# Kernel tuning notes

Measured on AMD Instinct MI355X. Metric: run time of the kernel, lower is better.

## Reference

```python
import jax, jax.numpy as jnp
import numpy as np

B, T, C = 4, 2048, 2048
H = 16
D = C // H  # head_dim = 128
THETA = 10000.0


def rope_cos_sin(t, d, dtype=jnp.float32):
    inv_freq = 1.0 / (THETA ** (jnp.arange(0, d, 2, dtype=jnp.float32) / d))  # [D/2]
    pos = jnp.arange(t, dtype=jnp.float32)
    freqs = jnp.outer(pos, inv_freq)                 # [T, D/2]
    emb = jnp.concatenate([freqs, freqs], axis=-1)   # [T, D]
    return jnp.cos(emb).astype(dtype), jnp.sin(emb).astype(dtype)


def rotate_half(x):
    x1, x2 = jnp.split(x, 2, axis=-1)
    return jnp.concatenate([-x2, x1], axis=-1)


def setup_inputs() -> dict:
    key = jax.random.key(0)
    k1, k2, k3 = jax.random.split(key, 3)
    x = jax.random.normal(k1, (B, T, C), dtype=jnp.float32)
    Wqkv = jax.random.normal(k2, (C, 3 * C), dtype=jnp.float32) * (1.0 / np.sqrt(C))
    Wout = jax.random.normal(k3, (C, C), dtype=jnp.float32) * (1.0 / np.sqrt(C))
    return {"x": x, "Wqkv": Wqkv, "Wout": Wout}


def reference(x, Wqkv, Wout):
    b, t, c = x.shape
    qkv = jnp.einsum('btc,cd->btd', x, Wqkv)          # [B,T,3C]
    q, k, v = jnp.split(qkv, 3, axis=-1)
    # [B,T,C] -> [B,H,T,D]
    q = q.reshape(b, t, H, D).transpose(0, 2, 1, 3)
    k = k.reshape(b, t, H, D).transpose(0, 2, 1, 3)
    v = v.reshape(b, t, H, D).transpose(0, 2, 1, 3)
    cos, sin = rope_cos_sin(t, D, x.dtype)            # [T,D]
    cos = cos[None, None]                             # [1,1,T,D]
    sin = sin[None, None]
    q = q * cos + rotate_half(q) * sin
    k = k * cos + rotate_half(k) * sin
    scale = 1.0 / np.sqrt(D)
    scores = jnp.einsum('bhqd,bhkd->bhqk', q, k) * scale
    causal = jnp.tril(jnp.ones((t, t), dtype=bool))
    scores = jnp.where(causal[None, None], scores, jnp.finfo(scores.dtype).min)
    attn = jax.nn.softmax(scores, axis=-1)
    y = jnp.einsum('bhqk,bhkd->bhqd', attn, v)        # [B,H,T,D]
    y = y.transpose(0, 2, 1, 3).reshape(b, t, c)      # [B,T,C]
    return jnp.einsum('btc,cd->btd', y, Wout)
```

## Files before the change

kernel.cpp:

```cpp
#include <hip/hip_runtime.h>
#include <hip/hip_bf16.h>
#include <cmath>

#define Bsz   4
#define Tlen  2048
#define Cdim  2048
#define Hn    16
#define Dh    128
#define N_QKV 6144
#define Mrows 8192

typedef __bf16 bf16x8 __attribute__((ext_vector_type(8)));
typedef __bf16 bf16x4 __attribute__((ext_vector_type(4)));
typedef float  f32x4  __attribute__((ext_vector_type(4)));
typedef uint32_t u32x2 __attribute__((ext_vector_type(2)));

__device__ __forceinline__ f32x4 mfma16(bf16x8 a, bf16x8 b, f32x4 c) {
  return __builtin_amdgcn_mfma_f32_16x16x32_bf16(a, b, c, 0, 0, 0);
}

__device__ __forceinline__ void gl16(const void* g, void* l) {
  __builtin_amdgcn_global_load_lds(
      (const __attribute__((address_space(1))) void*)g,
      (__attribute__((address_space(3))) void*)l, 16, 0, 0);
}

__device__ __forceinline__ uint32_t pack_bf16(float lo, float hi) {
  union { __bf16 h; unsigned short u; } a, b;
  a.h = (__bf16)lo; b.h = (__bf16)hi;
  return (uint32_t)a.u | ((uint32_t)b.u << 16);
}

__global__ void rope_table_k(float* __restrict__ cosT, float* __restrict__ sinT) {
  int idx = blockIdx.x * 256 + threadIdx.x;
  int t = idx >> 6, i = idx & 63;
  float invf = __expf(-(float)i * 0.14391156698f);
  float a = (float)t * invf;
  float s, c;
  sincosf(a, &s, &c);
  cosT[idx] = c;
  sinT[idx] = s;
}

__global__ __launch_bounds__(256) void f32_to_bf16_k(
    const float* __restrict__ src, __bf16* __restrict__ dst) {
  size_t i = ((size_t)blockIdx.x * 256 + threadIdx.x) * 8;
  f32x4 a = *(const f32x4*)(src + i);
  f32x4 b = *(const f32x4*)(src + i + 4);
  bf16x8 o;
  o[0] = (__bf16)a[0]; o[1] = (__bf16)a[1]; o[2] = (__bf16)a[2]; o[3] = (__bf16)a[3];
  o[4] = (__bf16)b[0]; o[5] = (__bf16)b[1]; o[6] = (__bf16)b[2]; o[7] = (__bf16)b[3];
  *(bf16x8*)(dst + i) = o;
}

__global__ __launch_bounds__(256) void transpose_to_bf16_k(
    const float* __restrict__ src, __bf16* __restrict__ dst, int K, int N) {
  __shared__ float tile[32][33];
  int n0 = blockIdx.x * 32, k0 = blockIdx.y * 32;
  int tr = threadIdx.x >> 3, tc = (threadIdx.x & 7) * 4;
  f32x4 v = *(const f32x4*)&src[(size_t)(k0 + tr) * N + n0 + tc];
  tile[tr][tc + 0] = v[0]; tile[tr][tc + 1] = v[1];
  tile[tr][tc + 2] = v[2]; tile[tr][tc + 3] = v[3];
  __syncthreads();
  bf16x4 w;
  w[0] = (__bf16)tile[tc + 0][tr];
  w[1] = (__bf16)tile[tc + 1][tr];
  w[2] = (__bf16)tile[tc + 2][tr];
  w[3] = (__bf16)tile[tc + 3][tr];
  *(bf16x4*)&dst[(size_t)(n0 + tr) * K + k0 + tc] = w;
}

__global__ __launch_bounds__(512, 2) void qkv_gemm(
    const __bf16* __restrict__ Xb, const __bf16* __restrict__ Wt,
    __bf16* __restrict__ Qo, __bf16* __restrict__ Ko, __bf16* __restrict__ Vo,
    const float* __restrict__ cosT, const float* __restrict__ sinT)
{
  __shared__ union SM {
    struct { __bf16 A[2][256 * 64]; __bf16 B[2][256 * 64]; } s;
    float C[64][265];
  } sm;

  const int tid = threadIdx.x, lane = tid & 63, wid = tid >> 6;
  const int g = lane >> 4, l16 = lane & 15;
  const int wr = wid >> 2, wc = wid & 3;

  const int bid = blockIdx.x;
  const int xcd = bid & 7, idx = bid >> 3;
  const int stl = idx >> 4, pos = idx & 15;
  const int m0 = (xcd * 4 + (pos >> 2)) * 256;
  const int n0 = (stl * 4 + (pos & 3)) * 256;

  const int srow = tid >> 3;
  const int schk = (tid & 7) ^ (srow & 7);
  const __bf16* gA = Xb + (size_t)(m0 + srow) * Cdim + schk * 8;
  const __bf16* gB = Wt + (size_t)(n0 + srow) * Cdim + schk * 8;
  const int ldst = wid * 512;

  f32x4 acc[8][4] = {};
  const int NT = Cdim / 64;

  #pragma unroll
  for (int r = 0; r < 4; ++r) {
    gl16(gA + (size_t)r * 64 * Cdim, &sm.s.A[0][r * 4096 + ldst]);
    gl16(gB + (size_t)r * 64 * Cdim, &sm.s.B[0][r * 4096 + ldst]);
  }
  #pragma unroll
  for (int r = 0; r < 4; ++r) {
    gl16(gA + 64 + (size_t)r * 64 * Cdim, &sm.s.A[1][r * 4096 + ldst]);
    gl16(gB + 64 + (size_t)r * 64 * Cdim, &sm.s.B[1][r * 4096 + ldst]);
  }

  for (int t = 0; t < NT; ++t) {
    const int p = t & 1;
    if (t < NT - 1) asm volatile("s_waitcnt vmcnt(8)" ::: "memory");
    else            asm volatile("s_waitcnt vmcnt(0)" ::: "memory");
    __builtin_amdgcn_s_barrier();
    __builtin_amdgcn_sched_barrier(0);

    #pragma unroll
    for (int kk = 0; kk < 2; ++kk) {
      bf16x8 a[8], b[4];
      const int ch = (((kk << 2) | g) ^ (l16 & 7)) * 8;
      #pragma unroll
      for (int f = 0; f < 8; ++f)
        a[f] = *(const bf16x8*)&sm.s.A[p][(wr * 128 + f * 16 + l16) * 64 + ch];
      #pragma unroll
      for (int n = 0; n < 4; ++n)
        b[n] = *(const bf16x8*)&sm.s.B[p][(wc * 64 + n * 16 + l16) * 64 + ch];
      #pragma unroll
      for (int f = 0; f < 8; ++f)
        #pragma unroll
        for (int n = 0; n < 4; ++n)
          acc[f][n] = mfma16(a[f], b[n], acc[f][n]);
    }

    __builtin_amdgcn_sched_barrier(0);
    asm volatile("s_waitcnt lgkmcnt(0)" ::: "memory");
    __builtin_amdgcn_s_barrier();

    if (t + 2 < NT) {
      const __bf16* pA = gA + (size_t)(t + 2) * 64;
      const __bf16* pB = gB + (size_t)(t + 2) * 64;
      #pragma unroll
      for (int r = 0; r < 4; ++r) {
        gl16(pA + (size_t)r * 64 * Cdim, &sm.s.A[p][r * 4096 + ldst]);
        gl16(pB + (size_t)r * 64 * Cdim, &sm.s.B[p][r * 4096 + ldst]);
      }
    }
  }

  const int sel = n0 >> 11;
  const int h0  = (n0 & 2047) >> 7;
  const int erow = tid >> 3, q = tid & 7;
  const int dlo = (q & 3) * 16;
  const int clo = (q >> 2) * 128 + dlo;
  const int vcol = tid >> 1, vth = tid & 1;

  #pragma unroll
  for (int rh = 0; rh < 4; ++rh) {
    if (wr == (rh >> 1)) {
      const int fb = (rh & 1) * 4;
      #pragma unroll
      for (int f2 = 0; f2 < 4; ++f2)
        #pragma unroll
        for (int n = 0; n < 4; ++n)
          #pragma unroll
          for (int r = 0; r < 4; ++r)
            sm.C[f2 * 16 + g * 4 + r][wc * 64 + n * 16 + l16] = acc[fb + f2][n][r];
    }
    __syncthreads();
    if (sel == 2) {
      const int hh = h0 + (vcol >> 7), d = vcol & 127;
      const int mb = m0 + rh * 64 + vth * 32;
      const int b_ = mb >> 11, tt = mb & 2047;
      __bf16* outp = Vo + (((size_t)(b_ * Hn + hh)) * Dh + d) * Tlen + tt;
      bf16x8 w[4];
      #pragma unroll
      for (int i = 0; i < 32; ++i)
        w[i >> 3][i & 7] = (__bf16)sm.C[vth * 32 + i][vcol];
      #pragma unroll
      for (int k = 0; k < 4; ++k) *(bf16x8*)&outp[k * 8] = w[k];
    } else {
      __bf16* dst = (sel == 0) ? Qo : Ko;
      const int m = m0 + rh * 64 + erow;
      const int b_ = m >> 11, t = m & 2047;
      __bf16* out = dst + (((size_t)(b_ * Hn + h0 + (q >> 2))) * Tlen + t) * Dh + dlo;
      const float* cb = cosT + t * 64 + dlo;
      const float* sb = sinT + t * 64 + dlo;
      bf16x8 o1[2], o2[2];
      #pragma unroll
      for (int i = 0; i < 16; ++i) {
        float v1 = sm.C[erow][clo + i];
        float v2 = sm.C[erow][clo + i + 64];
        float cs = cb[i], sn = sb[i];
        float r1 = v1 * cs - v2 * sn;
        float r2 = v2 * cs + v1 * sn;
        o1[i >> 3][i & 7] = (__bf16)r1;
        o2[i >> 3][i & 7] = (__bf16)r2;
      }
      *(bf16x8*)&out[0]  = o1[0];
      *(bf16x8*)&out[8]  = o1[1];
      *(bf16x8*)&out[64] = o2[0];
      *(bf16x8*)&out[72] = o2[1];
    }
    __syncthreads();
  }
}

__global__ __launch_bounds__(256, 2) void attn_fwd(
    const __bf16* __restrict__ Qg, const __bf16* __restrict__ Kg,
    const __bf16* __restrict__ Vtg, __bf16* __restrict__ Yg)
{
  __shared__ __bf16 Ks[2][64 * 128];
  __shared__ __bf16 Vt[2][128 * 64];
  __shared__ uint32_t Ps2[4][16 * 34 + 2];

  const int tid = threadIdx.x, lane = tid & 63, wid = tid >> 6;
  const int g = lane >> 4, l16 = lane & 15;
  const int qt = gridDim.x - 1 - blockIdx.x;
  const int q0 = qt * 64;
  const size_t bh = (size_t)blockIdx.z * Hn + blockIdx.y;
  const __bf16* Kbase = Kg + bh * ((size_t)Tlen * Dh);
  const __bf16* Vbase = Vtg + bh * ((size_t)Dh * Tlen);

  const int q_glob = q0 + wid * 16 + l16;

  bf16x8 aq[4];
  {
    const __bf16* qrow = Qg + (bh * Tlen + q_glob) * Dh;
    #pragma unroll
    for (int ks = 0; ks < 4; ++ks)
      aq[ks] = *(const bf16x8*)(qrow + ks * 32 + 8 * g);
  }

  float m_r = -1e30f, l_r = 0.f;
  f32x4 o[8] = {};
  const float k_e = 0.08838834764831845f * 1.4426950408889634f;

  const int NKV = qt + 1;

  const int krow = lane >> 4, kchk = lane & 15;
  const int vrow = lane >> 3, vchk = lane & 7;

#define STAGE_KV(kv0_, buf_)                                                    \
  {                                                                             \
    _Pragma("unroll")                                                           \
    for (int rr = 0; rr < 4; ++rr) {                                            \
      const int row = wid * 16 + rr * 4 + krow;                                 \
      const int sc = kchk ^ (row & 7);                                          \
      gl16(Kbase + (size_t)((kv0_) + row) * Dh + sc * 8,                        \
           &Ks[buf_][(wid * 16 + rr * 4) * 128]);                               \
    }                                                                           \
    _Pragma("unroll")                                                           \
    for (int rr = 0; rr < 4; ++rr) {                                            \
      const int row = wid * 32 + rr * 8 + vrow;                                 \
      const int sc = vchk ^ (row & 7);                                          \
      gl16(Vbase + (size_t)row * Tlen + (kv0_) + sc * 8,                        \
           &Vt[buf_][(wid * 32 + rr * 8) * 64]);                                \
    }                                                                           \
  }

  STAGE_KV(0, 0);

  for (int it = 0; it < NKV; ++it) {
    const int p = it & 1;
    if (it + 1 < NKV) {
      STAGE_KV((it + 1) * 64, (it + 1) & 1);
      asm volatile("s_waitcnt vmcnt(8)" ::: "memory");
    } else {
      asm volatile("s_waitcnt vmcnt(0)" ::: "memory");
    }
    __builtin_amdgcn_s_barrier();
    __builtin_amdgcn_sched_barrier(0);

    f32x4 s[4] = {};
    __builtin_amdgcn_s_setprio(1);
    #pragma unroll
    for (int ks = 0; ks < 4; ++ks) {
      const int ch = ((4 * ks + g) ^ (l16 & 7)) * 8;
      #pragma unroll
      for (int nf = 0; nf < 4; ++nf) {
        bf16x8 bk = *(const bf16x8*)&Ks[p][(nf * 16 + l16) * 128 + ch];
        s[nf] = mfma16(bk, aq[ks], s[nf]);
      }
    }
    __builtin_amdgcn_s_setprio(0);

    if (it == qt) {
      const int kvb = it * 64 + 4 * g;
      #pragma unroll
      for (int nf = 0; nf < 4; ++nf)
        #pragma unroll
        for (int r = 0; r < 4; ++r)
          if (kvb + nf * 16 + r > q_glob) s[nf][r] = -1e30f;
    }

    float mx = s[0][0];
    #pragma unroll
    for (int nf = 0; nf < 4; ++nf)
      #pragma unroll
      for (int r = 0; r < 4; ++r) mx = fmaxf(mx, s[nf][r]);
    mx = fmaxf(mx, __shfl_xor(mx, 16, 64));
    mx = fmaxf(mx, __shfl_xor(mx, 32, 64));

    if (__any(mx > m_r)) {
      const float mn = fmaxf(m_r, mx);
      const float al = exp2f((m_r - mn) * k_e);
      m_r = mn;
      l_r *= al;
      #pragma unroll
      for (int n2 = 0; n2 < 8; ++n2)
        #pragma unroll
        for (int r = 0; r < 4; ++r) o[n2][r] *= al;
    }

    const float mk = -m_r * k_e;
    float rs = 0.f;
    #pragma unroll
    for (int nf = 0; nf < 4; ++nf)
      #pragma unroll
      for (int r = 0; r < 4; ++r) {
        const float pv = exp2f(fmaf(s[nf][r], k_e, mk));
        s[nf][r] = pv;
        rs += pv;
      }
    rs += __shfl_xor(rs, 16, 64);
    rs += __shfl_xor(rs, 32, 64);
    l_r += rs;

    #pragma unroll
    for (int nf = 0; nf < 4; ++nf) {
      u32x2 wv;
      wv.x = pack_bf16(s[nf][0], s[nf][1]);
      wv.y = pack_bf16(s[nf][2], s[nf][3]);
      *(u32x2*)&Ps2[wid][l16 * 34 + nf * 8 + 2 * g] = wv;
    }
    asm volatile("s_waitcnt lgkmcnt(0)" ::: "memory");
    __builtin_amdgcn_sched_barrier(0);

    union { u32x2 h[2]; bf16x8 v; } pb0, pb1;
    pb0.h[0] = *(const u32x2*)&Ps2[wid][l16 * 34 + 4 * g];
    pb0.h[1] = *(const u32x2*)&Ps2[wid][l16 * 34 + 4 * g + 2];
    pb1.h[0] = *(const u32x2*)&Ps2[wid][l16 * 34 + 16 + 4 * g];
    pb1.h[1] = *(const u32x2*)&Ps2[wid][l16 * 34 + 16 + 4 * g + 2];

    const int c0 = (g ^ (l16 & 7)) * 8;
    const int c1 = ((4 + g) ^ (l16 & 7)) * 8;
    __builtin_amdgcn_s_setprio(1);
    #pragma unroll
    for (int n2 = 0; n2 < 8; ++n2) {
      bf16x8 vb0 = *(const bf16x8*)&Vt[p][(n2 * 16 + l16) * 64 + c0];
      bf16x8 vb1 = *(const bf16x8*)&Vt[p][(n2 * 16 + l16) * 64 + c1];
      o[n2] = mfma16(vb0, pb0.v, o[n2]);
      o[n2] = mfma16(vb1, pb1.v, o[n2]);
    }
    __builtin_amdgcn_s_setprio(0);

    asm volatile("s_waitcnt lgkmcnt(0)" ::: "memory");
    __builtin_amdgcn_sched_barrier(0);
    __builtin_amdgcn_s_barrier();
  }
#undef STAGE_KV

  const float inv = 1.0f / l_r;
  __bf16* yrow = Yg + ((size_t)(blockIdx.z * Tlen + q0 + wid * 16 + l16)) * Cdim
               + blockIdx.y * Dh;
  #pragma unroll
  for (int n2 = 0; n2 < 8; ++n2) {
    bf16x4 w;
    #pragma unroll
    for (int r = 0; r < 4; ++r) w[r] = (__bf16)(o[n2][r] * inv);
    *(bf16x4*)&yrow[n2 * 16 + 4 * g] = w;
  }
}

__global__ __launch_bounds__(512, 2) void out_gemm(
    const __bf16* __restrict__ Yb, const __bf16* __restrict__ Wt,
    float* __restrict__ O)
{
  __shared__ struct { __bf16 A[2][256 * 64]; __bf16 B[2][256 * 64]; } sm;

  const int tid = threadIdx.x, lane = tid & 63, wid = tid >> 6;
  const int g = lane >> 4, l16 = lane & 15;
  const int wr = wid >> 2, wc = wid & 3;

  const int bid = blockIdx.x;
  const int xcd = bid & 7, idx = bid >> 3;
  const int stl = idx >> 4, pos = idx & 15;
  const int m0 = (xcd * 4 + (pos >> 2)) * 256;
  const int n0 = (stl * 4 + (pos & 3)) * 256;

  const int srow = tid >> 3;
  const int schk = (tid & 7) ^ (srow & 7);
  const __bf16* gA = Yb + (size_t)(m0 + srow) * Cdim + schk * 8;
  const __bf16* gB = Wt + (size_t)(n0 + srow) * Cdim + schk * 8;
  const int ldst = wid * 512;

  f32x4 acc[8][4] = {};
  const int NT = Cdim / 64;

  #pragma unroll
  for (int r = 0; r < 4; ++r) {
    gl16(gA + (size_t)r * 64 * Cdim, &sm.A[0][r * 4096 + ldst]);
    gl16(gB + (size_t)r * 64 * Cdim, &sm.B[0][r * 4096 + ldst]);
  }
  #pragma unroll
  for (int r = 0; r < 4; ++r) {
    gl16(gA + 64 + (size_t)r * 64 * Cdim, &sm.A[1][r * 4096 + ldst]);
    gl16(gB + 64 + (size_t)r * 64 * Cdim, &sm.B[1][r * 4096 + ldst]);
  }

  for (int t = 0; t < NT; ++t) {
    const int p = t & 1;
    if (t < NT - 1) asm volatile("s_waitcnt vmcnt(8)" ::: "memory");
    else            asm volatile("s_waitcnt vmcnt(0)" ::: "memory");
    __builtin_amdgcn_s_barrier();
    __builtin_amdgcn_sched_barrier(0);

    #pragma unroll
    for (int kk = 0; kk < 2; ++kk) {
      bf16x8 a[8], b[4];
      const int ch = (((kk << 2) | g) ^ (l16 & 7)) * 8;
      #pragma unroll
      for (int f = 0; f < 8; ++f)
        a[f] = *(const bf16x8*)&sm.A[p][(wr * 128 + f * 16 + l16) * 64 + ch];
      #pragma unroll
      for (int n = 0; n < 4; ++n)
        b[n] = *(const bf16x8*)&sm.B[p][(wc * 64 + n * 16 + l16) * 64 + ch];
      #pragma unroll
      for (int f = 0; f < 8; ++f)
        #pragma unroll
        for (int n = 0; n < 4; ++n)
          acc[f][n] = mfma16(a[f], b[n], acc[f][n]);
    }

    __builtin_amdgcn_sched_barrier(0);
    asm volatile("s_waitcnt lgkmcnt(0)" ::: "memory");
    __builtin_amdgcn_s_barrier();

    if (t + 2 < NT) {
      const __bf16* pA = gA + (size_t)(t + 2) * 64;
      const __bf16* pB = gB + (size_t)(t + 2) * 64;
      #pragma unroll
      for (int r = 0; r < 4; ++r) {
        gl16(pA + (size_t)r * 64 * Cdim, &sm.A[p][r * 4096 + ldst]);
        gl16(pB + (size_t)r * 64 * Cdim, &sm.B[p][r * 4096 + ldst]);
      }
    }
  }

  #pragma unroll
  for (int f = 0; f < 8; ++f)
    #pragma unroll
    for (int n = 0; n < 4; ++n)
      #pragma unroll
      for (int r = 0; r < 4; ++r)
        O[(size_t)(m0 + wr * 128 + f * 16 + g * 4 + r) * Cdim
          + (n0 + wc * 64 + n * 16 + l16)] = acc[f][n][r];
}

extern "C" void kernel_launch(void* const* d_in, const int* in_sizes, int n_in,
                              void* d_out, int out_size, void* d_ws, size_t ws_size,
                              hipStream_t stream) {
  const float* x    = (const float*)d_in[0];
  const float* Wqkv = (const float*)d_in[1];
  const float* Wout = (const float*)d_in[2];
  float* out = (float*)d_out;

  float*  cosT   = (float*)d_ws;
  float*  sinT   = cosT + Tlen * 64;
  __bf16* Xb     = (__bf16*)(sinT + Tlen * 64);
  __bf16* Wqkv_t = Xb + (size_t)Mrows * Cdim;
  __bf16* Wout_t = Wqkv_t + (size_t)N_QKV * Cdim;
  __bf16* Qb     = Wout_t + (size_t)Cdim * Cdim;
  __bf16* Kb     = Qb + (size_t)Bsz * Hn * Tlen * Dh;
  __bf16* Vb     = Kb + (size_t)Bsz * Hn * Tlen * Dh;
  __bf16* Yb     = Xb;

  rope_table_k<<<dim3(512), dim3(256), 0, stream>>>(cosT, sinT);
  f32_to_bf16_k<<<dim3(Mrows * Cdim / (256 * 8)), dim3(256), 0, stream>>>(x, Xb);
  transpose_to_bf16_k<<<dim3(N_QKV / 32, Cdim / 32), dim3(256), 0, stream>>>(
      Wqkv, Wqkv_t, Cdim, N_QKV);
  transpose_to_bf16_k<<<dim3(Cdim / 32, Cdim / 32), dim3(256), 0, stream>>>(
      Wout, Wout_t, Cdim, Cdim);
  qkv_gemm<<<dim3(768), dim3(512), 0, stream>>>(
      Xb, Wqkv_t, Qb, Kb, Vb, cosT, sinT);
  attn_fwd<<<dim3(Tlen / 64, Hn, Bsz), dim3(256), 0, stream>>>(Qb, Kb, Vb, Yb);
  out_gemm<<<dim3(256), dim3(512), 0, stream>>>(Yb, Wout_t, out);
}
```

Baseline: 670.0 us.

## Split GEMM k-tiles into quadrant phases with interleaved loads and MFMA priority

Both the QKV and output GEMMs now break each 64-wide k-tile into four sub-phases over quadrants of the 256x256 output tile. Each phase issues a quarter of the next tile's global-to-LDS loads, reads its A/B fragments, and runs its MFMAs under raised wave priority (s_setprio). The aim is to overlap memory traffic and LDS reads with matrix math more finely than the old whole-tile loop, and to lower register pressure from fragment arrays. In exchange it adds more barriers per k-tile, and the hand-scheduled vmcnt counts must line up exactly with the staged loads.

Measured after the change: 1.276 ms. 1.91x slower.

```diff
diff --git a/kernel.cpp b/kernel.cpp
--- a/kernel.cpp
+++ b/kernel.cpp
@@ -30,6 +30,51 @@
   a.h = (__bf16)lo; b.h = (__bf16)hi;
   return (uint32_t)a.u | ((uint32_t)b.u << 16);
 }
+
+union GemmSM {
+  struct { __bf16 A[2][256 * 64]; __bf16 B[2][256 * 64]; } s;
+  float C[64][265];
+};
+
+#define STAGE_A(buf_, k0_, mq_) {                                             \
+  _Pragma("unroll") for (int rnd_ = 0; rnd_ < 2; ++rnd_) {                    \
+    const int lr_ = rnd_ * 128 + (mq_) * 64 + (wid << 3);                     \
+    gl16(gA0 + (size_t)lr_ * Cdim + (k0_), &sm.s.A[buf_][lr_ * 64]);          \
+  } }
+#define STAGE_B(buf_, k0_, nq_) {                                             \
+  _Pragma("unroll") for (int rnd_ = 0; rnd_ < 2; ++rnd_) {                    \
+    const int lr_ = rnd_ * 128 + (nq_) * 32 + ((wid >> 2) << 6)               \
+                  + ((wid & 3) << 3);                                         \
+    gl16(gB0 + (size_t)lr_ * Cdim + (k0_), &sm.s.B[buf_][lr_ * 64]);          \
+  } }
+#define PHASE(buf_, mq_, nq_, VM_, STAGE_)                                    \
+  {                                                                           \
+    bf16x8 a_[4][2], b_[2][2];                                                \
+    _Pragma("unroll") for (int kk = 0; kk < 2; ++kk) {                        \
+      const int ch_ = (((kk << 2) | g) ^ (l16 & 7)) * 8;                      \
+      _Pragma("unroll") for (int fq = 0; fq < 4; ++fq)                        \
+        a_[fq][kk] = *(const bf16x8*)                                         \
+          &sm.s.A[buf_][(wr * 128 + (mq_) * 64 + fq * 16 + l16) * 64 + ch_];  \
+      _Pragma("unroll") for (int nn = 0; nn < 2; ++nn)                        \
+        b_[nn][kk] = *(const bf16x8*)                                         \
+          &sm.s.B[buf_][(wc * 64 + (nq_) * 32 + nn * 16 + l16) * 64 + ch_];   \
+    }                                                                         \
+    STAGE_                                                                    \
+    __builtin_amdgcn_s_barrier();                                             \
+    asm volatile("s_waitcnt lgkmcnt(0)" ::: "memory");                        \
+    __builtin_amdgcn_sched_barrier(0);                                        \
+    __builtin_amdgcn_s_setprio(1);                                            \
+    _Pragma("unroll") for (int kk = 0; kk < 2; ++kk)                          \
+      _Pragma("unroll") for (int fq = 0; fq < 4; ++fq)                        \
+        _Pragma("unroll") for (int nn = 0; nn < 2; ++nn)                      \
+          acc[(mq_) * 4 + fq][(nq_) * 2 + nn] =                               \
+            mfma16(a_[fq][kk], b_[nn][kk], acc[(mq_) * 4 + fq][(nq_) * 2 + nn]); \
+    __builtin_amdgcn_s_setprio(0);                                            \
+    __builtin_amdgcn_sched_barrier(0);                                        \
+    asm volatile("s_waitcnt vmcnt(" VM_ ")" ::: "memory");                    \
+    __builtin_amdgcn_s_barrier();                                             \
+    __builtin_amdgcn_sched_barrier(0);                                        \
+  }
 
 __global__ void rope_table_k(float* __restrict__ cosT, float* __restrict__ sinT) {
   int idx = blockIdx.x * 256 + threadIdx.x;
@@ -75,10 +120,7 @@
     __bf16* __restrict__ Qo, __bf16* __restrict__ Ko, __bf16* __restrict__ Vo,
     const float* __restrict__ cosT, const float* __restrict__ sinT)
 {
-  __shared__ union SM {
-    struct { __bf16 A[2][256 * 64]; __bf16 B[2][256 * 64]; } s;
-    float C[64][265];
-  } sm;
+  __shared__ GemmSM sm;
 
   const int tid = threadIdx.x, lane = tid & 63, wid = tid >> 6;
   const int g = lane >> 4, l16 = lane & 15;
@@ -90,63 +132,38 @@
   const int m0 = (xcd * 4 + (pos >> 2)) * 256;
   const int n0 = (stl * 4 + (pos & 3)) * 256;
 
-  const int srow = tid >> 3;
-  const int schk = (tid & 7) ^ (srow & 7);
-  const __bf16* gA = Xb + (size_t)(m0 + srow) * Cdim + schk * 8;
-  const __bf16* gB = Wt + (size_t)(n0 + srow) * Cdim + schk * 8;
-  const int ldst = wid * 512;
+  const int schk = (lane & 7) ^ ((lane >> 3) & 7);
+  const __bf16* gA0 = Xb + (size_t)(m0 + (lane >> 3)) * Cdim + schk * 8;
+  const __bf16* gB0 = Wt + (size_t)(n0 + (lane >> 3)) * Cdim + schk * 8;
 
   f32x4 acc[8][4] = {};
-  const int NT = Cdim / 64;
-
-  #pragma unroll
-  for (int r = 0; r < 4; ++r) {
-    gl16(gA + (size_t)r * 64 * Cdim, &sm.s.A[0][r * 4096 + ldst]);
-    gl16(gB + (size_t)r * 64 * Cdim, &sm.s.B[0][r * 4096 + ldst]);
-  }
-  #pragma unroll
-  for (int r = 0; r < 4; ++r) {
-    gl16(gA + 64 + (size_t)r * 64 * Cdim, &sm.s.A[1][r * 4096 + ldst]);
-    gl16(gB + 64 + (size_t)r * 64 * Cdim, &sm.s.B[1][r * 4096 + ldst]);
-  }
-
-  for (int t = 0; t < NT; ++t) {
-    const int p = t & 1;
-    if (t < NT - 1) asm volatile("s_waitcnt vmcnt(8)" ::: "memory");
-    else            asm volatile("s_waitcnt vmcnt(0)" ::: "memory");
-    __builtin_amdgcn_s_barrier();
-    __builtin_amdgcn_sched_barrier(0);
-
-    #pragma unroll
-    for (int kk = 0; kk < 2; ++kk) {
-      bf16x8 a[8], b[4];
-      const int ch = (((kk << 2) | g) ^ (l16 & 7)) * 8;
-      #pragma unroll
-      for (int f = 0; f < 8; ++f)
-        a[f] = *(const bf16x8*)&sm.s.A[p][(wr * 128 + f * 16 + l16) * 64 + ch];
-      #pragma unroll
-      for (int n = 0; n < 4; ++n)
-        b[n] = *(const bf16x8*)&sm.s.B[p][(wc * 64 + n * 16 + l16) * 64 + ch];
-      #pragma unroll
-      for (int f = 0; f < 8; ++f)
-        #pragma unroll
-        for (int n = 0; n < 4; ++n)
-          acc[f][n] = mfma16(a[f], b[n], acc[f][n]);
-    }
-
-    __builtin_amdgcn_sched_barrier(0);
-    asm volatile("s_waitcnt lgkmcnt(0)" ::: "memory");
-    __builtin_amdgcn_s_barrier();
-
-    if (t + 2 < NT) {
-      const __bf16* pA = gA + (size_t)(t + 2) * 64;
-      const __bf16* pB = gB + (size_t)(t + 2) * 64;
-      #pragma unroll
-      for (int r = 0; r < 4; ++r) {
-        gl16(pA + (size_t)r * 64 * Cdim, &sm.s.A[p][r * 4096 + ldst]);
-        gl16(pB + (size_t)r * 64 * Cdim, &sm.s.B[p][r * 4096 + ldst]);
-      }
-    }
+
+  STAGE_A(0, 0, 0) STAGE_B(0, 0, 0) STAGE_A(0, 0, 1) STAGE_B(0, 0, 1)
+  asm volatile("s_waitcnt vmcnt(4)" ::: "memory");
+  __builtin_amdgcn_s_barrier();
+  __builtin_amdgcn_sched_barrier(0);
+
+  for (int I = 0; I < 15; ++I) {
+    const int t1k = (2 * I + 1) * 64, t2k = (2 * I + 2) * 64;
+    PHASE(0, 0, 0, "4", STAGE_A(1, t1k, 0))
+    PHASE(0, 1, 0, "4", STAGE_B(1, t1k, 0))
+    PHASE(0, 0, 1, "4", STAGE_A(1, t1k, 1))
+    PHASE(0, 1, 1, "4", STAGE_B(1, t1k, 1))
+    PHASE(1, 0, 0, "4", STAGE_A(0, t2k, 0))
+    PHASE(1, 1, 0, "4", STAGE_B(0, t2k, 0))
+    PHASE(1, 0, 1, "4", STAGE_A(0, t2k, 1))
+    PHASE(1, 1, 1, "4", STAGE_B(0, t2k, 1))
+  }
+  {
+    const int t1k = 31 * 64;
+    PHASE(0, 0, 0, "4", STAGE_A(1, t1k, 0))
+    PHASE(0, 1, 0, "4", STAGE_B(1, t1k, 0))
+    PHASE(0, 0, 1, "4", STAGE_A(1, t1k, 1))
+    PHASE(0, 1, 1, "0", STAGE_B(1, t1k, 1))
+    PHASE(1, 0, 0, "0", )
+    PHASE(1, 1, 0, "0", )
+    PHASE(1, 0, 1, "0", )
+    PHASE(1, 1, 1, "0", )
   }
 
   const int sel = n0 >> 11;
@@ -378,7 +395,7 @@
     const __bf16* __restrict__ Yb, const __bf16* __restrict__ Wt,
     float* __restrict__ O)
 {
-  __shared__ struct { __bf16 A[2][256 * 64]; __bf16 B[2][256 * 64]; } sm;
+  __shared__ GemmSM sm;
 
   const int tid = threadIdx.x, lane = tid & 63, wid = tid >> 6;
   const int g = lane >> 4, l16 = lane & 15;
@@ -390,63 +407,38 @@
   const int m0 = (xcd * 4 + (pos >> 2)) * 256;
   const int n0 = (stl * 4 + (pos & 3)) * 256;
 
-  const int srow = tid >> 3;
-  const int schk = (tid & 7) ^ (srow & 7);
-  const __bf16* gA = Yb + (size_t)(m0 + srow) * Cdim + schk * 8;
-  const __bf16* gB = Wt + (size_t)(n0 + srow) * Cdim + schk * 8;
-  const int ldst = wid * 512;
+  const int schk = (lane & 7) ^ ((lane >> 3) & 7);
+  const __bf16* gA0 = Yb + (size_t)(m0 + (lane >> 3)) * Cdim + schk * 8;
+  const __bf16* gB0 = Wt + (size_t)(n0 + (lane >> 3)) * Cdim + schk * 8;
 
   f32x4 acc[8][4] = {};
-  const int NT = Cdim / 64;
-
-  #pragma unroll
-  for (int r = 0; r < 4; ++r) {
-    gl16(gA + (size_t)r * 64 * Cdim, &sm.A[0][r * 4096 + ldst]);
-    gl16(gB + (size_t)r * 64 * Cdim, &sm.B[0][r * 4096 + ldst]);
-  }
-  #pragma unroll
-  for (int r = 0; r < 4; ++r) {
-    gl16(gA + 64 + (size_t)r * 64 * Cdim, &sm.A[1][r * 4096 + ldst]);
-    gl16(gB + 64 + (size_t)r * 64 * Cdim, &sm.B[1][r * 4096 + ldst]);
-  }
-
-  for (int t = 0; t < NT; ++t) {
-    const int p = t & 1;
-    if (t < NT - 1) asm volatile("s_waitcnt vmcnt(8)" ::: "memory");
-    else            asm volatile("s_waitcnt vmcnt(0)" ::: "memory");
-    __builtin_amdgcn_s_barrier();
-    __builtin_amdgcn_sched_barrier(0);
-
-    #pragma unroll
-    for (int kk = 0; kk < 2; ++kk) {
-      bf16x8 a[8], b[4];
-      const int ch = (((kk << 2) | g) ^ (l16 & 7)) * 8;
-      #pragma unroll
-      for (int f = 0; f < 8; ++f)
-        a[f] = *(const bf16x8*)&sm.A[p][(wr * 128 + f * 16 + l16) * 64 + ch];
-      #pragma unroll
-      for (int n = 0; n < 4; ++n)
-        b[n] = *(const bf16x8*)&sm.B[p][(wc * 64 + n * 16 + l16) * 64 + ch];
-      #pragma unroll
-      for (int f = 0; f < 8; ++f)
-        #pragma unroll
-        for (int n = 0; n < 4; ++n)
-          acc[f][n] = mfma16(a[f], b[n], acc[f][n]);
-    }
-
-    __builtin_amdgcn_sched_barrier(0);
-    asm volatile("s_waitcnt lgkmcnt(0)" ::: "memory");
-    __builtin_amdgcn_s_barrier();
-
-    if (t + 2 < NT) {
-      const __bf16* pA = gA + (size_t)(t + 2) * 64;
-      const __bf16* pB = gB + (size_t)(t + 2) * 64;
-      #pragma unroll
-      for (int r = 0; r < 4; ++r) {
-        gl16(pA + (size_t)r * 64 * Cdim, &sm.A[p][r * 4096 + ldst]);
-        gl16(pB + (size_t)r * 64 * Cdim, &sm.B[p][r * 4096 + ldst]);
-      }
-    }
+
+  STAGE_A(0, 0, 0) STAGE_B(0, 0, 0) STAGE_A(0, 0, 1) STAGE_B(0, 0, 1)
+  asm volatile("s_waitcnt vmcnt(4)" ::: "memory");
+  __builtin_amdgcn_s_barrier();
+  __builtin_amdgcn_sched_barrier(0);
+
+  for (int I = 0; I < 15; ++I) {
+    const int t1k = (2 * I + 1) * 64, t2k = (2 * I + 2) * 64;
+    PHASE(0, 0, 0, "4", STAGE_A(1, t1k, 0))
+    PHASE(0, 1, 0, "4", STAGE_B(1, t1k, 0))
+    PHASE(0, 0, 1, "4", STAGE_A(1, t1k, 1))
+    PHASE(0, 1, 1, "4", STAGE_B(1, t1k, 1))
+    PHASE(1, 0, 0, "4", STAGE_A(0, t2k, 0))
+    PHASE(1, 1, 0, "4", STAGE_B(0, t2k, 0))
+    PHASE(1, 0, 1, "4", STAGE_A(0, t2k, 1))
+    PHASE(1, 1, 1, "4", STAGE_B(0, t2k, 1))
+  }
+  {
+    const int t1k = 31 * 64;
+    PHASE(0, 0, 0, "4", STAGE_A(1, t1k, 0))
+    PHASE(0, 1, 0, "4", STAGE_B(1, t1k, 0))
+    PHASE(0, 0, 1, "4", STAGE_A(1, t1k, 1))
+    PHASE(0, 1, 1, "0", STAGE_B(1, t1k, 1))
+    PHASE(1, 0, 0, "0", )
+    PHASE(1, 1, 0, "0", )
+    PHASE(1, 0, 1, "0", )
+    PHASE(1, 1, 1, "0", )
   }
 
   #pragma unroll
```

## Replace 256x256 double-buffered GEMMs with simpler 128x128 single-buffer tiles

Applied to the files above, without the earlier changes.

Both the QKV and output GEMMs move from 256x256 tiles with 512 threads, a two-stage global_load_lds pipeline and K-step 64 to 128x128 tiles with 256 threads, a single LDS buffer and K-step 32, with a barrier before and after every load. The grids grow to 3072 and 1024 blocks and the RoPE/V-transpose epilogue is remapped to one head per tile. Smaller tiles raise occupancy and parallelism, but they lower arithmetic intensity and remove the load/compute overlap, so the GEMMs become more exposed to memory latency.

Result: slower. 816.7 us (+21.9%).

```diff
diff --git a/kernel.cpp b/kernel.cpp
--- a/kernel.cpp
+++ b/kernel.cpp
@@ -70,110 +70,78 @@
   *(bf16x4*)&dst[(size_t)(n0 + tr) * K + k0 + tc] = w;
 }
 
-__global__ __launch_bounds__(512, 2) void qkv_gemm(
+__global__ __launch_bounds__(256) void qkv_gemm(
     const __bf16* __restrict__ Xb, const __bf16* __restrict__ Wt,
     __bf16* __restrict__ Qo, __bf16* __restrict__ Ko, __bf16* __restrict__ Vo,
     const float* __restrict__ cosT, const float* __restrict__ sinT)
 {
   __shared__ union SM {
-    struct { __bf16 A[2][256 * 64]; __bf16 B[2][256 * 64]; } s;
-    float C[64][265];
+    struct { __bf16 A[128 * 32]; __bf16 B[128 * 32]; } s;
+    float C[64][132];
   } sm;
 
   const int tid = threadIdx.x, lane = tid & 63, wid = tid >> 6;
   const int g = lane >> 4, l16 = lane & 15;
-  const int wr = wid >> 2, wc = wid & 3;
+  const int wr = wid >> 1, wc = wid & 1;
 
   const int bid = blockIdx.x;
   const int xcd = bid & 7, idx = bid >> 3;
-  const int stl = idx >> 4, pos = idx & 15;
-  const int m0 = (xcd * 4 + (pos >> 2)) * 256;
-  const int n0 = (stl * 4 + (pos & 3)) * 256;
-
-  const int srow = tid >> 3;
-  const int schk = (tid & 7) ^ (srow & 7);
-  const __bf16* gA = Xb + (size_t)(m0 + srow) * Cdim + schk * 8;
-  const __bf16* gB = Wt + (size_t)(n0 + srow) * Cdim + schk * 8;
-  const int ldst = wid * 512;
-
-  f32x4 acc[8][4] = {};
-  const int NT = Cdim / 64;
+  const int stl = idx >> 6, pos = idx & 63;
+  const int by = xcd * 8 + (pos >> 3), bx = stl * 8 + (pos & 7);
+  const int m0 = by * 128, n0 = bx * 128;
+
+  const int sr0 = lane >> 2;
+  f32x4 acc[4][4] = {};
+
+  for (int k0 = 0; k0 < Cdim; k0 += 32) {
+    __syncthreads();
+    #pragma unroll
+    for (int j = 0; j < 2; ++j) {
+      const int rr = wid * 32 + j * 16 + sr0;
+      const int sc = (lane & 3) ^ ((rr >> 1) & 3);
+      gl16(Xb + (size_t)(m0 + rr) * Cdim + k0 + sc * 8,
+           &sm.s.A[(wid * 32 + j * 16) * 32]);
+      gl16(Wt + (size_t)(n0 + rr) * Cdim + k0 + sc * 8,
+           &sm.s.B[(wid * 32 + j * 16) * 32]);
+    }
+    __syncthreads();
+
+    bf16x8 a[4], b[4];
+    const int ca = (g ^ ((l16 >> 1) & 3)) * 8;
+    #pragma unroll
+    for (int f = 0; f < 4; ++f) {
+      a[f] = *(const bf16x8*)&sm.s.A[(wr * 64 + f * 16 + l16) * 32 + ca];
+      b[f] = *(const bf16x8*)&sm.s.B[(wc * 64 + f * 16 + l16) * 32 + ca];
+    }
+    #pragma unroll
+    for (int mf = 0; mf < 4; ++mf)
+      #pragma unroll
+      for (int nf = 0; nf < 4; ++nf)
+        acc[mf][nf] = mfma16(a[mf], b[nf], acc[mf][nf]);
+  }
+
+  const int sel = n0 >> 11;
+  const int h   = (n0 & 2047) >> 7;
+  const int erow = tid >> 2, jb = (tid & 3) * 16;
+  const int vcol = tid >> 1, vth = tid & 1;
 
   #pragma unroll
-  for (int r = 0; r < 4; ++r) {
-    gl16(gA + (size_t)r * 64 * Cdim, &sm.s.A[0][r * 4096 + ldst]);
-    gl16(gB + (size_t)r * 64 * Cdim, &sm.s.B[0][r * 4096 + ldst]);
-  }
-  #pragma unroll
-  for (int r = 0; r < 4; ++r) {
-    gl16(gA + 64 + (size_t)r * 64 * Cdim, &sm.s.A[1][r * 4096 + ldst]);
-    gl16(gB + 64 + (size_t)r * 64 * Cdim, &sm.s.B[1][r * 4096 + ldst]);
-  }
-
-  for (int t = 0; t < NT; ++t) {
-    const int p = t & 1;
-    if (t < NT - 1) asm volatile("s_waitcnt vmcnt(8)" ::: "memory");
-    else            asm volatile("s_waitcnt vmcnt(0)" ::: "memory");
-    __builtin_amdgcn_s_barrier();
-    __builtin_amdgcn_sched_barrier(0);
-
-    #pragma unroll
-    for (int kk = 0; kk < 2; ++kk) {
-      bf16x8 a[8], b[4];
-      const int ch = (((kk << 2) | g) ^ (l16 & 7)) * 8;
-      #pragma unroll
-      for (int f = 0; f < 8; ++f)
-        a[f] = *(const bf16x8*)&sm.s.A[p][(wr * 128 + f * 16 + l16) * 64 + ch];
-      #pragma unroll
-      for (int n = 0; n < 4; ++n)
-        b[n] = *(const bf16x8*)&sm.s.B[p][(wc * 64 + n * 16 + l16) * 64 + ch];
-      #pragma unroll
-      for (int f = 0; f < 8; ++f)
+  for (int rh = 0; rh < 2; ++rh) {
+    __syncthreads();
+    if (wr == rh) {
+      #pragma unroll
+      for (int mf = 0; mf < 4; ++mf)
         #pragma unroll
-        for (int n = 0; n < 4; ++n)
-          acc[f][n] = mfma16(a[f], b[n], acc[f][n]);
-    }
-
-    __builtin_amdgcn_sched_barrier(0);
-    asm volatile("s_waitcnt lgkmcnt(0)" ::: "memory");
-    __builtin_amdgcn_s_barrier();
-
-    if (t + 2 < NT) {
-      const __bf16* pA = gA + (size_t)(t + 2) * 64;
-      const __bf16* pB = gB + (size_t)(t + 2) * 64;
-      #pragma unroll
-      for (int r = 0; r < 4; ++r) {
-        gl16(pA + (size_t)r * 64 * Cdim, &sm.s.A[p][r * 4096 + ldst]);
-        gl16(pB + (size_t)r * 64 * Cdim, &sm.s.B[p][r * 4096 + ldst]);
-      }
-    }
-  }
-
-  const int sel = n0 >> 11;
-  const int h0  = (n0 & 2047) >> 7;
-  const int erow = tid >> 3, q = tid & 7;
-  const int dlo = (q & 3) * 16;
-  const int clo = (q >> 2) * 128 + dlo;
-  const int vcol = tid >> 1, vth = tid & 1;
-
-  #pragma unroll
-  for (int rh = 0; rh < 4; ++rh) {
-    if (wr == (rh >> 1)) {
-      const int fb = (rh & 1) * 4;
-      #pragma unroll
-      for (int f2 = 0; f2 < 4; ++f2)
-        #pragma unroll
-        for (int n = 0; n < 4; ++n)
+        for (int nf = 0; nf < 4; ++nf)
           #pragma unroll
           for (int r = 0; r < 4; ++r)
-            sm.C[f2 * 16 + g * 4 + r][wc * 64 + n * 16 + l16] = acc[fb + f2][n][r];
+            sm.C[mf * 16 + g * 4 + r][wc * 64 + nf * 16 + l16] = acc[mf][nf][r];
     }
     __syncthreads();
     if (sel == 2) {
-      const int hh = h0 + (vcol >> 7), d = vcol & 127;
       const int mb = m0 + rh * 64 + vth * 32;
       const int b_ = mb >> 11, tt = mb & 2047;
-      __bf16* outp = Vo + (((size_t)(b_ * Hn + hh)) * Dh + d) * Tlen + tt;
+      __bf16* outp = Vo + (((size_t)(b_ * Hn + h)) * Dh + vcol) * Tlen + tt;
       bf16x8 w[4];
       #pragma unroll
       for (int i = 0; i < 32; ++i)
@@ -184,26 +152,25 @@
       __bf16* dst = (sel == 0) ? Qo : Ko;
       const int m = m0 + rh * 64 + erow;
       const int b_ = m >> 11, t = m & 2047;
-      __bf16* out = dst + (((size_t)(b_ * Hn + h0 + (q >> 2))) * Tlen + t) * Dh + dlo;
-      const float* cb = cosT + t * 64 + dlo;
-      const float* sb = sinT + t * 64 + dlo;
+      __bf16* out = dst + (((size_t)(b_ * Hn + h)) * Tlen + t) * Dh;
+      const float* cb = cosT + t * 64 + jb;
+      const float* sb = sinT + t * 64 + jb;
       bf16x8 o1[2], o2[2];
       #pragma unroll
       for (int i = 0; i < 16; ++i) {
-        float v1 = sm.C[erow][clo + i];
-        float v2 = sm.C[erow][clo + i + 64];
+        float v1 = sm.C[erow][jb + i];
+        float v2 = sm.C[erow][jb + i + 64];
         float cs = cb[i], sn = sb[i];
         float r1 = v1 * cs - v2 * sn;
         float r2 = v2 * cs + v1 * sn;
         o1[i >> 3][i & 7] = (__bf16)r1;
         o2[i >> 3][i & 7] = (__bf16)r2;
       }
-      *(bf16x8*)&out[0]  = o1[0];
-      *(bf16x8*)&out[8]  = o1[1];
-      *(bf16x8*)&out[64] = o2[0];
-      *(bf16x8*)&out[72] = o2[1];
-    }
-    __syncthreads();
+      *(bf16x8*)&out[jb]      = o1[0];
+      *(bf16x8*)&out[jb + 8]  = o1[1];
+      *(bf16x8*)&out[jb + 64] = o2[0];
+      *(bf16x8*)&out[jb + 72] = o2[1];
+    }
   }
 }
 
@@ -374,89 +341,60 @@
   }
 }
 
-__global__ __launch_bounds__(512, 2) void out_gemm(
+__global__ __launch_bounds__(256) void out_gemm(
     const __bf16* __restrict__ Yb, const __bf16* __restrict__ Wt,
     float* __restrict__ O)
 {
-  __shared__ struct { __bf16 A[2][256 * 64]; __bf16 B[2][256 * 64]; } sm;
+  __shared__ struct { __bf16 A[128 * 32]; __bf16 B[128 * 32]; } sm;
 
   const int tid = threadIdx.x, lane = tid & 63, wid = tid >> 6;
   const int g = lane >> 4, l16 = lane & 15;
-  const int wr = wid >> 2, wc = wid & 3;
+  const int wr = wid >> 1, wc = wid & 1;
 
   const int bid = blockIdx.x;
   const int xcd = bid & 7, idx = bid >> 3;
-  const int stl = idx >> 4, pos = idx & 15;
-  const int m0 = (xcd * 4 + (pos >> 2)) * 256;
-  const int n0 = (stl * 4 + (pos & 3)) * 256;
-
-  const int srow = tid >> 3;
-  const int schk = (tid & 7) ^ (srow & 7);
-  const __bf16* gA = Yb + (size_t)(m0 + srow) * Cdim + schk * 8;
-  const __bf16* gB = Wt + (size_t)(n0 + srow) * Cdim + schk * 8;
-  const int ldst = wid * 512;
-
-  f32x4 acc[8][4] = {};
-  const int NT = Cdim / 64;
+  const int stl = idx >> 6, pos = idx & 63;
+  const int by = xcd * 8 + (pos >> 3), bx = stl * 8 + (pos & 7);
+  const int m0 = by * 128, n0 = bx * 128;
+
+  const int sr0 = lane >> 2;
+  f32x4 acc[4][4] = {};
+
+  for (int k0 = 0; k0 < Cdim; k0 += 32) {
+    __syncthreads();
+    #pragma unroll
+    for (int j = 0; j < 2; ++j) {
+      const int rr = wid * 32 + j * 16 + sr0;
+      const int sc = (lane & 3) ^ ((rr >> 1) & 3);
+      gl16(Yb + (size_t)(m0 + rr) * Cdim + k0 + sc * 8,
+           &sm.A[(wid * 32 + j * 16) * 32]);
+      gl16(Wt + (size_t)(n0 + rr) * Cdim + k0 + sc * 8,
+           &sm.B[(wid * 32 + j * 16) * 32]);
+    }
+    __syncthreads();
+
+    bf16x8 a[4], b[4];
+    const int ca = (g ^ ((l16 >> 1) & 3)) * 8;
+    #pragma unroll
+    for (int f = 0; f < 4; ++f) {
+      a[f] = *(const bf16x8*)&sm.A[(wr * 64 + f * 16 + l16) * 32 + ca];
+      b[f] = *(const bf16x8*)&sm.B[(wc * 64 + f * 16 + l16) * 32 + ca];
+    }
+    #pragma unroll
+    for (int mf = 0; mf < 4; ++mf)
+      #pragma unroll
+      for (int nf = 0; nf < 4; ++nf)
+        acc[mf][nf] = mfma16(a[mf], b[nf], acc[mf][nf]);
+  }
 
   #pragma unroll
-  for (int r = 0; r < 4; ++r) {
-    gl16(gA + (size_t)r * 64 * Cdim, &sm.A[0][r * 4096 + ldst]);
-    gl16(gB + (size_t)r * 64 * Cdim, &sm.B[0][r * 4096 + ldst]);
-  }
-  #pragma unroll
-  for (int r = 0; r < 4; ++r) {
-    gl16(gA + 64 + (size_t)r * 64 * Cdim, &sm.A[1][r * 4096 + ldst]);
-    gl16(gB + 64 + (size_t)r * 64 * Cdim, &sm.B[1][r * 4096 + ldst]);
-  }
-
-  for (int t = 0; t < NT; ++t) {
-    const int p = t & 1;
-    if (t < NT - 1) asm volatile("s_waitcnt vmcnt(8)" ::: "memory");
-    else            asm volatile("s_waitcnt vmcnt(0)" ::: "memory");
-    __builtin_amdgcn_s_barrier();
-    __builtin_amdgcn_sched_barrier(0);
-
-    #pragma unroll
-    for (int kk = 0; kk < 2; ++kk) {
-      bf16x8 a[8], b[4];
-      const int ch = (((kk << 2) | g) ^ (l16 & 7)) * 8;
-      #pragma unroll
-      for (int f = 0; f < 8; ++f)
-        a[f] = *(const bf16x8*)&sm.A[p][(wr * 128 + f * 16 + l16) * 64 + ch];
-      #pragma unroll
-      for (int n = 0; n < 4; ++n)
-        b[n] = *(const bf16x8*)&sm.B[p][(wc * 64 + n * 16 + l16) * 64 + ch];
-      #pragma unroll
-      for (int f = 0; f < 8; ++f)
-        #pragma unroll
-        for (int n = 0; n < 4; ++n)
-          acc[f][n] = mfma16(a[f], b[n], acc[f][n]);
-    }
-
-    __builtin_amdgcn_sched_barrier(0);
-    asm volatile("s_waitcnt lgkmcnt(0)" ::: "memory");
-    __builtin_amdgcn_s_barrier();
-
-    if (t + 2 < NT) {
-      const __bf16* pA = gA + (size_t)(t + 2) * 64;
-      const __bf16* pB = gB + (size_t)(t + 2) * 64;
-      #pragma unroll
-      for (int r = 0; r < 4; ++r) {
-        gl16(pA + (size_t)r * 64 * Cdim, &sm.A[p][r * 4096 + ldst]);
-        gl16(pB + (size_t)r * 64 * Cdim, &sm.B[p][r * 4096 + ldst]);
-      }
-    }
-  }
-
-  #pragma unroll
-  for (int f = 0; f < 8; ++f)
-    #pragma unroll
-    for (int n = 0; n < 4; ++n)
+  for (int mf = 0; mf < 4; ++mf)
+    #pragma unroll
+    for (int nf = 0; nf < 4; ++nf)
       #pragma unroll
       for (int r = 0; r < 4; ++r)
-        O[(size_t)(m0 + wr * 128 + f * 16 + g * 4 + r) * Cdim
-          + (n0 + wc * 64 + n * 16 + l16)] = acc[f][n][r];
+        O[(size_t)(m0 + wr * 64 + mf * 16 + g * 4 + r) * Cdim
+          + (n0 + wc * 64 + nf * 16 + l16)] = acc[mf][nf][r];
 }
 
 extern "C" void kernel_launch(void* const* d_in, const int* in_sizes, int n_in,
@@ -483,8 +421,8 @@
       Wqkv, Wqkv_t, Cdim, N_QKV);
   transpose_to_bf16_k<<<dim3(Cdim / 32, Cdim / 32), dim3(256), 0, stream>>>(
       Wout, Wout_t, Cdim, Cdim);
-  qkv_gemm<<<dim3(768), dim3(512), 0, stream>>>(
+  qkv_gemm<<<dim3(3072), dim3(256), 0, stream>>>(
       Xb, Wqkv_t, Qb, Kb, Vb, cosT, sinT);
   attn_fwd<<<dim3(Tlen / 64, Hn, Bsz), dim3(256), 0, stream>>>(Qb, Kb, Vb, Yb);
-  out_gemm<<<dim3(256), dim3(512), 0, stream>>>(Yb, Wout_t, out);
-}
+  out_gemm<<<dim3(1024), dim3(256), 0, stream>>>(Yb, Wout_t, out);
+}
```
